# Kernel tuning notes

Measured on AMD Instinct MI355X. Metric: run time of the kernel, lower is better.

The kernel has to match this reference:

```python
import jax, jax.numpy as jnp
import numpy as np

B, N, STRIDE, NSAMPLE, RADIUS = 2, 8192, 4, 32, 0.1
CIN, COUT, LPC = 64, 128, 16
M = N // STRIDE
EPS = 1e-5


def conv1d(x, W, b=None):
    y = jnp.einsum('oc,bcn->bon', W, x)
    return y + b[None, :, None] if b is not None else y


def conv2d(x, W, b=None):
    y = jnp.einsum('oc,bcmk->bomk', W, x)
    return y + b[None, :, None, None] if b is not None else y


def bn(x, prm):
    # prm: [4, C] = (gamma, beta, running_mean, running_var); inference BN
    sh = (1, -1) + (1,) * (x.ndim - 2)
    g, be, m, v = (prm[i].reshape(sh) for i in range(4))
    return (x - m) * jax.lax.rsqrt(v + EPS) * g + be


def fps(p, m):
    # furthest point sampling, p: [B,N,3] -> idx [B,m] int32 (starts at index 0)
    b, n, _ = p.shape
    first = jnp.zeros((b,), jnp.int32)
    d0 = jnp.full((b, n), 1e10, p.dtype)

    def step(carry, _):
        dist, last = carry
        lastp = jnp.take_along_axis(p, jnp.broadcast_to(last[:, None, None], (b, 1, 3)), axis=1)
        dist = jnp.minimum(dist, jnp.sum((p - lastp) ** 2, -1))
        nxt = jnp.argmax(dist, -1).astype(jnp.int32)
        return (dist, nxt), nxt

    _, rest = jax.lax.scan(step, (d0, first), None, length=m - 1)
    return jnp.concatenate([first[:, None], rest.T], axis=1)


def ball_query(q, s, radius, ns):
    # q [B,M,3], s [B,N,3] -> neighbor indices [B,M,ns] (first ns points within radius, padded with first hit)
    n = s.shape[1]
    sqd = jnp.sum((q[:, :, None, :] - s[:, None, :, :]) ** 2, -1)  # [B,M,N]
    cand = jnp.where(sqd < radius * radius, jnp.arange(n, dtype=jnp.int32)[None, None, :], n)
    srt = jnp.sort(cand, axis=-1)[:, :, :ns]
    first = srt[:, :, :1]
    return jnp.where(srt == n, first, srt)


def group(feat, gidx):
    # feat [B,C,N], gidx [B,M,ns] -> [B,C,M,ns]
    return jax.vmap(lambda ft, gi: ft[:, gi])(feat, gidx)


def setup_inputs() -> dict:
    key = jax.random.key(0)
    ks = jax.random.split(key, 24)

    def w(k_, o, i):
        return jax.random.normal(k_, (o, i), jnp.float32) / np.sqrt(i).astype(np.float32)

    def bnp(k_, c):  # positive gamma/var, small-ish beta/mean
        return jax.random.uniform(k_, (4, c), jnp.float32) + 0.1

    return {
        'p': jax.random.uniform(ks[0], (B, N, 3), jnp.float32),
        'lp': jax.random.normal(ks[1], (B, LPC, N), jnp.float32),
        'f': jax.random.normal(ks[2], (B, CIN, N), jnp.float32),
        'W_skip': w(ks[3], COUT, CIN), 'b_skip': jax.random.normal(ks[4], (COUT,), jnp.float32) * 0.02,
        'W_post': w(ks[5], COUT, CIN), 'bn_post': bnp(ks[6], COUT),
        'W_loc1': w(ks[7], 32, LPC), 'bn_loc1': bnp(ks[8], 32),
        'W_loc2': w(ks[9], COUT, 32), 'bn_loc2': bnp(ks[10], COUT),
        'W_g': w(ks[11], 1, CIN), 'b_g': jax.random.normal(ks[12], (1,), jnp.float32) * 0.02,
        'W_v': w(ks[13], CIN, CIN), 'b_v': jax.random.normal(ks[14], (CIN,), jnp.float32) * 0.02,
        'W_w1': w(ks[15], CIN // 4, CIN), 'bn_w1': bnp(ks[16], CIN // 4),
        'W_w2': w(ks[17], CIN, CIN // 4), 'b_w2': jax.random.normal(ks[18], (CIN,), jnp.float32) * 0.02,
        'W_m': w(ks[19], COUT, CIN), 'bn_m': bnp(ks[20], COUT),
    }


def reference(p, lp, f, W_skip, b_skip, W_post, bn_post, W_loc1, bn_loc1, W_loc2, bn_loc2,
              W_g, b_g, W_v, b_v, W_w1, bn_w1, W_w2, b_w2, W_m, bn_m):
    b, n = p.shape[0], p.shape[1]
    m = n // STRIDE
    relu = jax.nn.relu

    # --- sampling + gathers ---
    idx = fps(p, m)  # [B,M]
    new_p = jnp.take_along_axis(p, jnp.broadcast_to(idx[:, :, None], (b, m, 3)), axis=1)
    fi = jnp.take_along_axis(f, jnp.broadcast_to(idx[:, None, :], (b, f.shape[1], m)), axis=2)
    lpi = jnp.take_along_axis(lp, jnp.broadcast_to(idx[:, None, :], (b, lp.shape[1], m)), axis=2)
    identity = conv1d(fi, W_skip, b_skip)  # [B,COUT,M]

    # --- global top-k relative-position attention branch ---
    att = jax.nn.sigmoid(conv1d(fi, W_g, b_g))  # [B,1,M]
    k = min(m // 4, 160)
    _, index_k = jax.lax.top_k(att[:, 0, :], k)  # [B,k]
    sparse_f = jnp.take_along_axis(fi, jnp.broadcast_to(index_k[:, None, :], (b, fi.shape[1], k)), axis=2)
    v = conv1d(sparse_f, W_v, b_v)  # [B,CIN,k]
    fi_att = fi * att
    r_qk = fi_att[:, :, :, None] - sparse_f[:, :, None, :]  # [B,CIN,M,k]
    r_qk = relu(bn(conv2d(r_qk, W_w1), bn_w1))
    r_qk = conv2d(r_qk, W_w2, b_w2)
    w_ = relu(r_qk)
    attfeat = jnp.mean(w_ * v[:, :, None, :], axis=-1)  # [B,CIN,M]
    global_f = relu(bn(conv1d(attfeat - fi, W_m), bn_m))  # [B,COUT,M]

    # --- local grouping branch ---
    fpost = relu(bn(conv1d(f, W_post), bn_post))  # [B,COUT,N]
    lpf = jnp.concatenate([lp, fpost], axis=1)  # [B,LPC+COUT,N]
    gidx = ball_query(new_p, p, RADIUS, NSAMPLE)  # [B,M,ns]
    lpfj = group(lpf, gidx)  # [B,LPC+COUT,M,ns]
    lpj, fj = lpfj[:, :LPC], lpfj[:, LPC:]
    dlpj = lpj - lpi[:, :, :, None]
    loc = relu(bn(conv2d(dlpj, W_loc1), bn_loc1))
    loc = relu(bn(conv2d(loc, W_loc2), bn_loc2))
    fout = jnp.max(fj + loc, axis=-1)  # [B,COUT,M]
    fout = fout + global_f
    fout = relu(fout + identity)
    return new_p, lpi, fout
```

## Files before the change

### kernel.cpp

```cpp
#include <hip/hip_runtime.h>
#include <stdint.h>

#define BB 2
#define NN 8192
#define MM 2048
#define CIN_ 64
#define COUT_ 128
#define LPC_ 16
#define NS_ 32
#define KSEL 160
#define EPSB 1e-5f

#define WS_IDX    0
#define WS_IDXK   4096
#define WS_LOGIT  4416
#define WS_ATT    8512
#define WS_FLAG   16380
#define WS_FIT    16384
#define WS_IDT    278528
#define WS_A1S    802816
#define WS_VT     868352
#define WS_B1S    888832
#define WS_GFT    893952
#define WS_FPOST  1418240
#define WS_GIDX   3515392

#define OUT_NEWP 0
#define OUT_LPI  12288
#define OUT_F    77824

typedef float    f16v __attribute__((ext_vector_type(16)));
typedef unsigned u16v __attribute__((ext_vector_type(16)));
typedef int      i16v __attribute__((ext_vector_type(16)));
typedef unsigned u8v  __attribute__((ext_vector_type(8)));

__device__ __forceinline__ float dist2_rn(float ax, float ay, float az,
                                          float bx, float by, float bz) {
  float dx = __fsub_rn(ax, bx);
  float dy = __fsub_rn(ay, by);
  float dz = __fsub_rn(az, bz);
  return __fadd_rn(__fadd_rn(__fmul_rn(dx, dx), __fmul_rn(dy, dy)), __fmul_rn(dz, dz));
}

template <int CTRL>
__device__ __forceinline__ unsigned long long dppmax64(unsigned long long x) {
  unsigned lo = (unsigned)x, hi = (unsigned)(x >> 32);
  unsigned plo = (unsigned)__builtin_amdgcn_update_dpp(0, (int)lo, CTRL, 0xF, 0xF, true);
  unsigned phi = (unsigned)__builtin_amdgcn_update_dpp(0, (int)hi, CTRL, 0xF, 0xF, true);
  unsigned long long o = ((unsigned long long)phi << 32) | plo;
  return o > x ? o : x;
}
#define DPP_XOR1 0xB1
#define DPP_XOR2 0x4E
#define DPP_HALFMIR 0x141
#define DPP_MIR 0x140
#define DPP_BC15 0x142
#define DPP_BC31 0x143

__device__ __forceinline__ unsigned mort4(unsigned x) {
  return (x & 1u) | ((x & 2u) << 2) | ((x & 4u) << 4) | ((x & 8u) << 6);
}

#define PPT 16
#define FPS_T 512
#define NWAVE 8
#define FPOST_BLKS ((BB * NN * 16) / FPS_T)
#define WARM_BLKS 254
#define WARM_CAP 32768
#define ANCHOR_CAP 8192

__global__ __launch_bounds__(FPS_T) void k_fps_fpost(const float* __restrict__ p,
                                                     int* __restrict__ idx_out,
                                                     const float* __restrict__ f,
                                                     const float* __restrict__ Wpost,
                                                     const float* __restrict__ bnpost,
                                                     float* __restrict__ fpostT,
                                                     int* __restrict__ flag) {
  __shared__ float2 xyl[NN];
  __shared__ union UZ {
    float zz[NN];
    struct { float zlow[NN - 4096]; unsigned short perm[NN]; } s;
  } uz;
  __shared__ union UH {
    unsigned int hist[4096];
    int idxs[MM];
  } uh;
  __shared__ unsigned long long slots[2][NWAVE];
  __shared__ unsigned int wsum[NWAVE];

  if (blockIdx.x >= 2 + FPOST_BLKS) {
    if (blockIdx.x == 2 + FPOST_BLKS) {
      float a = 1.0000001f, acc = (float)threadIdx.x;
      for (int it = 0; it < ANCHOR_CAP; ++it) {
        if (__hip_atomic_load(flag, __ATOMIC_RELAXED, __HIP_MEMORY_SCOPE_AGENT) >= 2) break;
        #pragma unroll 64
        for (int k = 0; k < 512; ++k) acc = __builtin_fmaf(acc, a, 1.0f);
      }
      asm volatile("" ::"v"(acc));
    } else {
      for (int it = 0; it < WARM_CAP; ++it) {
        if (__hip_atomic_load(flag, __ATOMIC_RELAXED, __HIP_MEMORY_SCOPE_AGENT) >= 2) break;
        __builtin_amdgcn_s_sleep(8);
      }
    }
    return;
  }

  if (blockIdx.x >= 2) {
    int gt = (blockIdx.x - 2) * FPS_T + threadIdx.x;
    int og = gt & 15, nn = gt >> 4;
    int b = nn >> 13, n = nn & 8191;
    const float* fb = f + b * CIN_ * NN + n;
    float acc[8];
    #pragma unroll
    for (int q = 0; q < 8; q++) acc[q] = 0.f;
    for (int c = 0; c < 64; c++) {
      float x = fb[c * NN];
      #pragma unroll
      for (int q = 0; q < 8; q++) acc[q] = fmaf(Wpost[(og * 8 + q) * 64 + c], x, acc[q]);
    }
    #pragma unroll
    for (int q = 0; q < 8; q++) {
      int o = og * 8 + q;
      float ga = bnpost[o], be = bnpost[COUT_ + o], mu = bnpost[2 * COUT_ + o],
            va = bnpost[3 * COUT_ + o];
      float sc = ga / sqrtf(va + EPSB);
      fpostT[(b * NN + n) * 128 + o] = fmaxf(acc[q] * sc + (be - mu * sc), 0.f);
    }
    return;
  }

  const int b = blockIdx.x;
  if (threadIdx.x == 0)
    __hip_atomic_store(flag, 0, __ATOMIC_RELAXED, __HIP_MEMORY_SCOPE_AGENT);
  const float* pb = p + b * NN * 3;
  const int tid = threadIdx.x;
  const int lane = tid & 63;
  const int wid = tid >> 6;

  for (int i = tid; i < 4096; i += FPS_T) uh.hist[i] = 0u;
  __syncthreads();

  i16v cellv;
  #pragma unroll
  for (int k = 0; k < PPT; k++) {
    int i = tid + k * FPS_T;
    float x = pb[i * 3 + 0], y = pb[i * 3 + 1], z = pb[i * 3 + 2];
    int cx = (int)(x * 16.f); cx = cx < 0 ? 0 : (cx > 15 ? 15 : cx);
    int cy = (int)(y * 16.f); cy = cy < 0 ? 0 : (cy > 15 ? 15 : cy);
    int cz = (int)(z * 16.f); cz = cz < 0 ? 0 : (cz > 15 ? 15 : cz);
    int c = (int)(mort4((unsigned)cx) | (mort4((unsigned)cy) << 1) |
                  (mort4((unsigned)cz) << 2));
    cellv[k] = c;
    atomicAdd(&uh.hist[c], 1u);
  }
  __syncthreads();

  u8v h;
  unsigned int s = 0;
  #pragma unroll
  for (int k = 0; k < 8; k++) { h[k] = uh.hist[tid * 8 + k]; s += h[k]; }
  unsigned int pre = s;
  for (int d = 1; d < 64; d <<= 1) {
    unsigned int o = (unsigned int)__shfl_up((int)pre, d);
    if (lane >= d) pre += o;
  }
  if (lane == 63) wsum[wid] = pre;
  __syncthreads();
  if (tid < NWAVE) {
    unsigned int v = wsum[tid];
    unsigned int q = v;
    for (int d = 1; d < NWAVE; d <<= 1) {
      unsigned int o = (unsigned int)__shfl_up((int)q, d);
      if (tid >= d) q += o;
    }
    wsum[tid] = q - v;
  }
  __syncthreads();
  unsigned int base = wsum[wid] + (pre - s);
  #pragma unroll
  for (int k = 0; k < 8; k++) {
    uh.hist[tid * 8 + k] = base;
    base += h[k];
  }
  __syncthreads();

  #pragma unroll
  for (int k = 0; k < PPT; k++) {
    unsigned int pos = atomicAdd(&uh.hist[cellv[k]], 1u);
    uz.s.perm[pos] = (unsigned short)(tid + k * FPS_T);
  }
  __syncthreads();

  u16v porig;
  #pragma unroll
  for (int q = 0; q < PPT; q++) porig[q] = uz.s.perm[tid * PPT + q];
  __syncthreads();

  f16v dist;
  u16v lov;
  float bxmin = 1e30f, bymin = 1e30f, bzmin = 1e30f;
  float bxmax = -1e30f, bymax = -1e30f, bzmax = -1e30f;
  #pragma unroll
  for (int q = 0; q < PPT; q++) {
    unsigned int o = porig[q];
    float x = pb[o * 3 + 0], y = pb[o * 3 + 1], z = pb[o * 3 + 2];
    xyl[q * FPS_T + tid] = make_float2(x, y);
    uz.zz[q * FPS_T + tid] = z;
    lov[q] = ((8191u - o) << 13) | ((unsigned)tid << 4) | (unsigned)q;
    dist[q] = 1e10f;
    bxmin = fminf(bxmin, x); bxmax = fmaxf(bxmax, x);
    bymin = fminf(bymin, y); bymax = fmaxf(bymax, y);
    bzmin = fminf(bzmin, z); bzmax = fmaxf(bzmax, z);
  }

  float wx = pb[0], wy = pb[1], wz = pb[2];
  unsigned long long thrPack = ((unsigned long long)__float_as_uint(1e10f) << 32);
  __syncthreads();

  if (tid == 0) uh.idxs[0] = 0;

  for (int t = 1; t < MM; t++) {
    const int buf = t & 1;
    float ex = fmaxf(fmaxf(bxmin - wx, wx - bxmax), 0.f);
    float ey = fmaxf(fmaxf(bymin - wy, wy - bymax), 0.f);
    float ez = fmaxf(fmaxf(bzmin - wz, wz - bzmax), 0.f);
    float bd = (ex * ex + ey * ey + ez * ez) * 0.999f;
    float thrMax = __uint_as_float((unsigned int)(thrPack >> 32));
    bool active = (bd < thrMax);
    if (active) {
      unsigned long long m0 = 0ull, m1 = 0ull, m2 = 0ull, m3 = 0ull;
      #pragma unroll
      for (int q = 0; q < PPT; q++) {
        float2 a = xyl[q * FPS_T + tid];
        float az = uz.zz[q * FPS_T + tid];
        float d = dist2_rn(a.x, a.y, az, wx, wy, wz);
        float nd = fminf(dist[q], d);
        dist[q] = nd;
        unsigned long long pk =
            ((unsigned long long)__float_as_uint(nd) << 32) | (unsigned long long)lov[q];
        if ((q & 3) == 0) m0 = pk > m0 ? pk : m0;
        else if ((q & 3) == 1) m1 = pk > m1 ? pk : m1;
        else if ((q & 3) == 2) m2 = pk > m2 ? pk : m2;
        else m3 = pk > m3 ? pk : m3;
      }
      unsigned long long ba = m0 > m1 ? m0 : m1;
      unsigned long long bb2 = m2 > m3 ? m2 : m3;
      thrPack = ba > bb2 ? ba : bb2;
    }
    unsigned long long wp = thrPack;
    wp = dppmax64<DPP_XOR1>(wp);
    wp = dppmax64<DPP_XOR2>(wp);
    wp = dppmax64<DPP_HALFMIR>(wp);
    wp = dppmax64<DPP_MIR>(wp);
    wp = dppmax64<DPP_BC15>(wp);
    wp = dppmax64<DPP_BC31>(wp);
    unsigned wlo = (unsigned)__builtin_amdgcn_readlane((int)(unsigned)wp, 63);
    unsigned whi = (unsigned)__builtin_amdgcn_readlane((int)(unsigned)(wp >> 32), 63);
    unsigned long long wmax = ((unsigned long long)whi << 32) | wlo;
    if (thrPack == wmax) slots[buf][wid] = wmax;
    __syncthreads();

    int sidx = lane & (NWAVE - 1);
    unsigned long long w2 = slots[buf][sidx];
    w2 = dppmax64<DPP_XOR1>(w2);
    w2 = dppmax64<DPP_XOR2>(w2);
    w2 = dppmax64<DPP_HALFMIR>(w2);
    unsigned lo32 = (unsigned)w2;
    int tidwin = (int)((lo32 >> 4) & 511u);
    int qwin = (int)(lo32 & 15u);
    float2 cw = xyl[qwin * FPS_T + tidwin];
    float zw = uz.zz[qwin * FPS_T + tidwin];
    wx = cw.x; wy = cw.y; wz = zw;
    if (tid == 0) uh.idxs[t] = 8191 - (int)((lo32 >> 13) & 0x1FFFu);
  }
  __syncthreads();

  for (int i = tid; i < MM; i += FPS_T) idx_out[b * MM + i] = uh.idxs[i];
  __syncthreads();
  if (tid == 0)
    __hip_atomic_fetch_add(flag, 1, __ATOMIC_RELEASE, __HIP_MEMORY_SCOPE_AGENT);
}

__global__ __launch_bounds__(256) void k_gather(const float* __restrict__ p,
                                                const float* __restrict__ lp,
                                                const float* __restrict__ f,
                                                const int* __restrict__ idx,
                                                const float* __restrict__ Wg,
                                                const float* __restrict__ bg,
                                                float* __restrict__ fiT,
                                                float* __restrict__ logit,
                                                float* __restrict__ att,
                                                float* __restrict__ out_lpi,
                                                float* __restrict__ out_newp) {
  int gm = blockIdx.x * 256 + threadIdx.x;
  if (gm >= BB * MM) return;
  int b = gm >> 11, m = gm & 2047;
  int j = idx[gm];
  out_newp[gm * 3 + 0] = p[(b * NN + j) * 3 + 0];
  out_newp[gm * 3 + 1] = p[(b * NN + j) * 3 + 1];
  out_newp[gm * 3 + 2] = p[(b * NN + j) * 3 + 2];
  const float* lpb = lp + b * LPC_ * NN;
  float* olpi = out_lpi + b * LPC_ * MM;
  #pragma unroll
  for (int c = 0; c < LPC_; c++) olpi[c * MM + m] = lpb[c * NN + j];
  const float* fb = f + b * CIN_ * NN;
  float lg = bg[0];
  #pragma unroll
  for (int c = 0; c < CIN_; c++) {
    float x = fb[c * NN + j];
    fiT[gm * 64 + c] = x;
    lg = __fadd_rn(lg, __fmul_rn(Wg[c], x));
  }
  logit[gm] = lg;
  att[gm] = 1.f / (1.f + expf(-lg));
}

__global__ __launch_bounds__(256) void k_ident(const float* __restrict__ fiT,
                                               const float* __restrict__ Wskip,
                                               const float* __restrict__ bskip,
                                               float* __restrict__ idT) {
  int gt = blockIdx.x * 256 + threadIdx.x;
  if (gt >= BB * MM * 16) return;
  int og = gt & 15, gm = gt >> 4;
  const float* fvp = fiT + gm * 64;
  #pragma unroll
  for (int q = 0; q < 8; q++) {
    int o = og * 8 + q;
    float a = bskip[o];
    #pragma unroll
    for (int c = 0; c < 64; c++) a = fmaf(Wskip[o * 64 + c], fvp[c], a);
    idT[gm * 128 + o] = a;
  }
}

__global__ __launch_bounds__(1024) void k_topk(const float* __restrict__ att,
                                               int* __restrict__ idxk) {
  __shared__ unsigned long long key[MM];
  int b = blockIdx.x, tid = threadIdx.x;
  for (int i = tid; i < MM; i += 1024) {
    unsigned int u = __float_as_uint(att[b * MM + i]);
    u ^= (u & 0x80000000u) ? 0xFFFFFFFFu : 0x80000000u;
    u = ~u;
    key[i] = ((unsigned long long)u << 32) | (unsigned int)i;
  }
  __syncthreads();
  for (int k = 2; k <= MM; k <<= 1) {
    for (int j = k >> 1; j > 0; j >>= 1) {
      for (int i = tid; i < MM; i += 1024) {
        int ixj = i ^ j;
        if (ixj > i) {
          bool up = (i & k) == 0;
          unsigned long long a = key[i], c = key[ixj];
          if ((a > c) == up) { key[i] = c; key[ixj] = a; }
        }
      }
      __syncthreads();
    }
  }
  if (tid < KSEL) idxk[b * KSEL + tid] = (int)(key[tid] & 0xFFFFFFFFull);
}

__global__ __launch_bounds__(256) void k_a1s(const float* __restrict__ fiT,
                                             const float* __restrict__ att,
                                             const float* __restrict__ Ww1,
                                             const float* __restrict__ bnw1,
                                             float* __restrict__ a1sT) {
  int gm = blockIdx.x * 256 + threadIdx.x;
  if (gm >= BB * MM) return;
  const float* fvp = fiT + gm * 64;
  float a = att[gm];
  #pragma unroll
  for (int c1 = 0; c1 < 16; c1++) {
    float acc = 0.f;
    #pragma unroll
    for (int c = 0; c < 64; c++) acc = fmaf(Ww1[c1 * 64 + c], fvp[c] * a, acc);
    float g = bnw1[c1], be = bnw1[16 + c1], mu = bnw1[32 + c1], va = bnw1[48 + c1];
    float sc = g / sqrtf(va + EPSB);
    a1sT[gm * 16 + c1] = acc * sc + (be - mu * sc);
  }
}

__global__ __launch_bounds__(256) void k_vb1(const float* __restrict__ fiT,
                                             const int* __restrict__ idxk,
                                             const float* __restrict__ Wv,
                                             const float* __restrict__ bv,
                                             const float* __restrict__ Ww1,
                                             const float* __restrict__ bnw1,
                                             float* __restrict__ vT,
                                             float* __restrict__ b1sT) {
  int gk = blockIdx.x * 256 + threadIdx.x;
  if (gk >= BB * KSEL) return;
  int b = gk / KSEL;
  int kk = idxk[gk];
  const float* fvp = fiT + (b * MM + kk) * 64;
  for (int o = 0; o < 64; o++) {
    float acc = bv[o];
    #pragma unroll
    for (int c = 0; c < 64; c++) acc = fmaf(Wv[o * 64 + c], fvp[c], acc);
    vT[gk * 64 + o] = acc;
  }
  #pragma unroll
  for (int c1 = 0; c1 < 16; c1++) {
    float acc = 0.f;
    #pragma unroll
    for (int c = 0; c < 64; c++) acc = fmaf(Ww1[c1 * 64 + c], fvp[c], acc);
    float g = bnw1[c1], va = bnw1[48 + c1];
    b1sT[gk * 16 + c1] = acc * (g / sqrtf(va + EPSB));
  }
}

__global__ __launch_bounds__(256) void k_att(const float* __restrict__ a1sT,
                                             const float* __restrict__ b1sT,
                                             const float* __restrict__ vT,
                                             const float* __restrict__ fiT,
                                             const float* __restrict__ Ww2,
                                             const float* __restrict__ bw2,
                                             const float* __restrict__ Wm,
                                             const float* __restrict__ bnm,
                                             float* __restrict__ gfT) {
  __shared__ float B1sh[KSEL * 16];
  __shared__ float dsh[4][64];
  int b = blockIdx.x >> 9;
  const float* bsrc = b1sT + b * KSEL * 16;
  for (int i = threadIdx.x; i < KSEL * 16; i += 256) B1sh[i] = bsrc[i];
  __syncthreads();
  int wid = threadIdx.x >> 6, lane = threadIdx.x & 63;
  int gm = blockIdx.x * 4 + wid;
  int c15 = lane & 15;
  float a1 = a1sT[gm * 16 + c15];
  f16v wrow;
  #pragma unroll
  for (int c = 0; c < 16; c++) wrow[c] = Ww2[lane * 16 + c];
  float bw = bw2[lane];
  const float* vp = vT + b * KSEL * 64 + lane;
  float acc = 0.f;
  for (int k = 0; k < KSEL; k++) {
    float t = fmaxf(a1 - B1sh[k * 16 + c15], 0.f);
    float r2 = bw;
    #pragma unroll
    for (int c = 0; c < 16; c++) {
      float tc = __int_as_float(__builtin_amdgcn_readlane(__float_as_int(t), c));
      r2 = fmaf(wrow[c], tc, r2);
    }
    acc = fmaf(fmaxf(r2, 0.f), vp[k * 64], acc);
  }
  float af = acc * (1.f / (float)KSEL);
  float d = af - fiT[gm * 64 + lane];
  dsh[wid][lane] = d;
  __syncthreads();
  #pragma unroll
  for (int t2 = 0; t2 < 2; t2++) {
    int o = lane + t2 * 64;
    float g = 0.f;
    #pragma unroll
    for (int c = 0; c < 64; c++) g = fmaf(Wm[o * 64 + c], dsh[wid][c], g);
    float ga = bnm[o], be = bnm[COUT_ + o], mu = bnm[2 * COUT_ + o], va = bnm[3 * COUT_ + o];
    float sc = ga / sqrtf(va + EPSB);
    gfT[gm * 128 + o] = fmaxf(g * sc + (be - mu * sc), 0.f);
  }
}

__global__ __launch_bounds__(256) void k_ball(const float* __restrict__ p,
                                              const float* __restrict__ newp,
                                              int* __restrict__ gidx) {
  int wid = threadIdx.x >> 6, lane = threadIdx.x & 63;
  int gm = blockIdx.x * 4 + wid;
  int b = gm >> 11;
  const float* q = newp + gm * 3;
  float qx = q[0], qy = q[1], qz = q[2];
  const float* pb = p + b * NN * 3;
  int* out = gidx + gm * NS_;
  const float RR = (float)(0.1 * 0.1);
  int cnt = 0, firstj = 0;
  bool haveFirst = false;
  for (int chunk = 0; chunk < NN / 64 && cnt < NS_; chunk++) {
    int j = chunk * 64 + lane;
    float d = dist2_rn(qx, qy, qz, pb[j * 3], pb[j * 3 + 1], pb[j * 3 + 2]);
    unsigned long long mask = __ballot(d < RR);
    while (mask && cnt < NS_) {
      int l = __ffsll(mask) - 1;
      mask &= mask - 1;
      int jj = chunk * 64 + l;
      if (!haveFirst) { firstj = jj; haveFirst = true; }
      if (lane == 0) out[cnt] = jj;
      cnt++;
    }
  }
  if (lane == 0) {
    for (int i = cnt; i < NS_; i++) out[i] = firstj;
  }
}

__global__ __launch_bounds__(128) void k_final(const float* __restrict__ lp,
                                               const float* __restrict__ lpi_out,
                                               const int* __restrict__ gidx,
                                               const float* __restrict__ Wl1,
                                               const float* __restrict__ bnl1,
                                               const float* __restrict__ Wl2,
                                               const float* __restrict__ bnl2,
                                               const float* __restrict__ fpostT,
                                               const float* __restrict__ gfT,
                                               const float* __restrict__ idT,
                                               float* __restrict__ out_f) {
  __shared__ float loc1[NS_][32];
  __shared__ float dls[NS_][16];
  int gm = blockIdx.x;
  int b = gm >> 11, m = gm & 2047;
  int tid = threadIdx.x;
  const int* gx = gidx + gm * NS_;
  for (int i = tid; i < NS_ * 16; i += 128) {
    int s = i >> 4, c = i & 15;
    int j = gx[s];
    dls[s][c] = lp[(b * LPC_ + c) * NN + j] - lpi_out[(b * LPC_ + c) * MM + m];
  }
  __syncthreads();
  for (int i = tid; i < NS_ * 32; i += 128) {
    int s = i >> 5, o = i & 31;
    float a = 0.f;
    #pragma unroll
    for (int c = 0; c < 16; c++) a = fmaf(Wl1[o * 16 + c], dls[s][c], a);
    float ga = bnl1[o], be = bnl1[32 + o], mu = bnl1[64 + o], va = bnl1[96 + o];
    float sc = ga / sqrtf(va + EPSB);
    loc1[s][o] = fmaxf(a * sc + (be - mu * sc), 0.f);
  }
  __syncthreads();
  f16v wr0, wr1;
  #pragma unroll
  for (int c = 0; c < 16; c++) { wr0[c] = Wl2[tid * 32 + c]; wr1[c] = Wl2[tid * 32 + 16 + c]; }
  float ga = bnl2[tid], be = bnl2[128 + tid], mu = bnl2[256 + tid], va = bnl2[384 + tid];
  float sc = ga / sqrtf(va + EPSB);
  float sh = be - mu * sc;
  float mx = -1e30f;
  for (int s = 0; s < NS_; s++) {
    float g = 0.f;
    #pragma unroll
    for (int c = 0; c < 16; c++) g = fmaf(wr0[c], loc1[s][c], g);
    #pragma unroll
    for (int c = 0; c < 16; c++) g = fmaf(wr1[c], loc1[s][16 + c], g);
    float l2 = fmaxf(g * sc + sh, 0.f);
    int j = gx[s];
    float fj = fpostT[(b * NN + j) * 128 + tid];
    mx = fmaxf(mx, fj + l2);
  }
  float fout = fmaxf(mx + gfT[gm * 128 + tid] + idT[gm * 128 + tid], 0.f);
  out_f[(b * COUT_ + tid) * MM + m] = fout;
}

extern "C" void kernel_launch(void* const* d_in, const int* in_sizes, int n_in,
                              void* d_out, int out_size, void* d_ws, size_t ws_size,
                              hipStream_t stream) {
  (void)in_sizes; (void)n_in; (void)out_size; (void)ws_size;
  const float* p      = (const float*)d_in[0];
  const float* lp     = (const float*)d_in[1];
  const float* f      = (const float*)d_in[2];
  const float* W_skip = (const float*)d_in[3];
  const float* b_skip = (const float*)d_in[4];
  const float* W_post = (const float*)d_in[5];
  const float* bn_post= (const float*)d_in[6];
  const float* W_loc1 = (const float*)d_in[7];
  const float* bn_loc1= (const float*)d_in[8];
  const float* W_loc2 = (const float*)d_in[9];
  const float* bn_loc2= (const float*)d_in[10];
  const float* W_g    = (const float*)d_in[11];
  const float* b_g    = (const float*)d_in[12];
  const float* W_v    = (const float*)d_in[13];
  const float* b_v    = (const float*)d_in[14];
  const float* W_w1   = (const float*)d_in[15];
  const float* bn_w1  = (const float*)d_in[16];
  const float* W_w2   = (const float*)d_in[17];
  const float* b_w2   = (const float*)d_in[18];
  const float* W_m    = (const float*)d_in[19];
  const float* bn_m   = (const float*)d_in[20];

  float* out = (float*)d_out;
  float* ws = (float*)d_ws;
  int*   idx    = (int*)(ws + WS_IDX);
  int*   idxk   = (int*)(ws + WS_IDXK);
  float* att    = ws + WS_ATT;
  int*   flag   = (int*)(ws + WS_FLAG);
  float* fiT    = ws + WS_FIT;
  float* idT    = ws + WS_IDT;
  float* a1sT   = ws + WS_A1S;
  float* vT     = ws + WS_VT;
  float* b1sT   = ws + WS_B1S;
  float* gfT    = ws + WS_GFT;
  float* fpostT = ws + WS_FPOST;
  float* logit  = ws + WS_LOGIT;
  int*   gidx   = (int*)(ws + WS_GIDX);

  k_fps_fpost<<<2 + FPOST_BLKS + WARM_BLKS, FPS_T, 0, stream>>>(p, idx, f, W_post, bn_post,
                                                                fpostT, flag);
  k_gather<<<(BB * MM + 255) / 256, 256, 0, stream>>>(p, lp, f, idx, W_g, b_g, fiT, logit, att,
                                                      out + OUT_LPI, out + OUT_NEWP);
  k_ident<<<(BB * MM * 16) / 256, 256, 0, stream>>>(fiT, W_skip, b_skip, idT);
  k_topk<<<BB, 1024, 0, stream>>>(att, idxk);
  k_a1s<<<(BB * MM + 255) / 256, 256, 0, stream>>>(fiT, att, W_w1, bn_w1, a1sT);
  k_vb1<<<(BB * KSEL + 255) / 256, 256, 0, stream>>>(fiT, idxk, W_v, b_v, W_w1, bn_w1, vT, b1sT);
  k_att<<<(BB * MM) / 4, 256, 0, stream>>>(a1sT, b1sT, vT, fiT, W_w2, b_w2, W_m, bn_m, gfT);
  k_ball<<<(BB * MM) / 4, 256, 0, stream>>>(p, out + OUT_NEWP, gidx);
  k_final<<<BB * MM, 128, 0, stream>>>(lp, out + OUT_LPI, gidx, W_loc1, bn_loc1, W_loc2, bn_loc2,
                                       fpostT, gfT, idT, out + OUT_F);
}
```

Measured before the change: 2.335 ms.

## Fuse small kernels into gather, attention and final kernels to cut launches

Folds the a1s projection into the gather kernel, the skip/identity projection into the attention kernel, and the ball query into the final kernel, so k_ident, k_a1s and k_ball disappear. It removes three launches and the round trips of idT inputs, a1s inputs and gidx through global memory. The cost is that ball query now runs inside each 128-thread final block with only one wave active during the search, and the attention kernel does more per-thread work. The a1s computation now applies att after accumulation rather than per element, which changes rounding slightly.

```diff
diff --git a/kernel.cpp b/kernel.cpp
--- a/kernel.cpp
+++ b/kernel.cpp
@@ -13,7 +13,6 @@
 
 #define WS_IDX    0
 #define WS_IDXK   4096
-#define WS_LOGIT  4416
 #define WS_ATT    8512
 #define WS_FLAG   16380
 #define WS_FIT    16384
@@ -23,7 +22,6 @@
 #define WS_B1S    888832
 #define WS_GFT    893952
 #define WS_FPOST  1418240
-#define WS_GIDX   3515392
 
 #define OUT_NEWP 0
 #define OUT_LPI  12288
@@ -288,9 +286,11 @@
                                                 const int* __restrict__ idx,
                                                 const float* __restrict__ Wg,
                                                 const float* __restrict__ bg,
+                                                const float* __restrict__ Ww1,
+                                                const float* __restrict__ bnw1,
                                                 float* __restrict__ fiT,
-                                                float* __restrict__ logit,
                                                 float* __restrict__ att,
+                                                float* __restrict__ a1sT,
                                                 float* __restrict__ out_lpi,
                                                 float* __restrict__ out_newp) {
   int gm = blockIdx.x * 256 + threadIdx.x;
@@ -306,31 +306,23 @@
   for (int c = 0; c < LPC_; c++) olpi[c * MM + m] = lpb[c * NN + j];
   const float* fb = f + b * CIN_ * NN;
   float lg = bg[0];
-  #pragma unroll
+  f16v acc;
+  #pragma unroll
+  for (int c1 = 0; c1 < 16; c1++) acc[c1] = 0.f;
   for (int c = 0; c < CIN_; c++) {
     float x = fb[c * NN + j];
     fiT[gm * 64 + c] = x;
     lg = __fadd_rn(lg, __fmul_rn(Wg[c], x));
-  }
-  logit[gm] = lg;
-  att[gm] = 1.f / (1.f + expf(-lg));
-}
-
-__global__ __launch_bounds__(256) void k_ident(const float* __restrict__ fiT,
-                                               const float* __restrict__ Wskip,
-                                               const float* __restrict__ bskip,
-                                               float* __restrict__ idT) {
-  int gt = blockIdx.x * 256 + threadIdx.x;
-  if (gt >= BB * MM * 16) return;
-  int og = gt & 15, gm = gt >> 4;
-  const float* fvp = fiT + gm * 64;
-  #pragma unroll
-  for (int q = 0; q < 8; q++) {
-    int o = og * 8 + q;
-    float a = bskip[o];
-    #pragma unroll
-    for (int c = 0; c < 64; c++) a = fmaf(Wskip[o * 64 + c], fvp[c], a);
-    idT[gm * 128 + o] = a;
+    #pragma unroll
+    for (int c1 = 0; c1 < 16; c1++) acc[c1] = fmaf(Ww1[c1 * 64 + c], x, acc[c1]);
+  }
+  float a = 1.f / (1.f + expf(-lg));
+  att[gm] = a;
+  #pragma unroll
+  for (int c1 = 0; c1 < 16; c1++) {
+    float g = bnw1[c1], be = bnw1[16 + c1], mu = bnw1[32 + c1], va = bnw1[48 + c1];
+    float sc = g / sqrtf(va + EPSB);
+    a1sT[gm * 16 + c1] = (acc[c1] * a) * sc + (be - mu * sc);
   }
 }
 
@@ -359,26 +351,6 @@
     }
   }
   if (tid < KSEL) idxk[b * KSEL + tid] = (int)(key[tid] & 0xFFFFFFFFull);
-}
-
-__global__ __launch_bounds__(256) void k_a1s(const float* __restrict__ fiT,
-                                             const float* __restrict__ att,
-                                             const float* __restrict__ Ww1,
-                                             const float* __restrict__ bnw1,
-                                             float* __restrict__ a1sT) {
-  int gm = blockIdx.x * 256 + threadIdx.x;
-  if (gm >= BB * MM) return;
-  const float* fvp = fiT + gm * 64;
-  float a = att[gm];
-  #pragma unroll
-  for (int c1 = 0; c1 < 16; c1++) {
-    float acc = 0.f;
-    #pragma unroll
-    for (int c = 0; c < 64; c++) acc = fmaf(Ww1[c1 * 64 + c], fvp[c] * a, acc);
-    float g = bnw1[c1], be = bnw1[16 + c1], mu = bnw1[32 + c1], va = bnw1[48 + c1];
-    float sc = g / sqrtf(va + EPSB);
-    a1sT[gm * 16 + c1] = acc * sc + (be - mu * sc);
-  }
 }
 
 __global__ __launch_bounds__(256) void k_vb1(const float* __restrict__ fiT,
@@ -418,9 +390,13 @@
                                              const float* __restrict__ bw2,
                                              const float* __restrict__ Wm,
                                              const float* __restrict__ bnm,
-                                             float* __restrict__ gfT) {
+                                             const float* __restrict__ Wskip,
+                                             const float* __restrict__ bskip,
+                                             float* __restrict__ gfT,
+                                             float* __restrict__ idT) {
   __shared__ float B1sh[KSEL * 16];
   __shared__ float dsh[4][64];
+  __shared__ float fish[4][64];
   int b = blockIdx.x >> 9;
   const float* bsrc = b1sT + b * KSEL * 16;
   for (int i = threadIdx.x; i < KSEL * 16; i += 256) B1sh[i] = bsrc[i];
@@ -429,6 +405,8 @@
   int gm = blockIdx.x * 4 + wid;
   int c15 = lane & 15;
   float a1 = a1sT[gm * 16 + c15];
+  float fval = fiT[gm * 64 + lane];
+  fish[wid][lane] = fval;
   f16v wrow;
   #pragma unroll
   for (int c = 0; c < 16; c++) wrow[c] = Ww2[lane * 16 + c];
@@ -446,55 +424,29 @@
     acc = fmaf(fmaxf(r2, 0.f), vp[k * 64], acc);
   }
   float af = acc * (1.f / (float)KSEL);
-  float d = af - fiT[gm * 64 + lane];
+  float d = af - fval;
   dsh[wid][lane] = d;
   __syncthreads();
   #pragma unroll
   for (int t2 = 0; t2 < 2; t2++) {
     int o = lane + t2 * 64;
     float g = 0.f;
+    float ida = bskip[o];
     #pragma unroll
     for (int c = 0; c < 64; c++) g = fmaf(Wm[o * 64 + c], dsh[wid][c], g);
+    #pragma unroll
+    for (int c = 0; c < 64; c++) ida = fmaf(Wskip[o * 64 + c], fish[wid][c], ida);
     float ga = bnm[o], be = bnm[COUT_ + o], mu = bnm[2 * COUT_ + o], va = bnm[3 * COUT_ + o];
     float sc = ga / sqrtf(va + EPSB);
     gfT[gm * 128 + o] = fmaxf(g * sc + (be - mu * sc), 0.f);
-  }
-}
-
-__global__ __launch_bounds__(256) void k_ball(const float* __restrict__ p,
-                                              const float* __restrict__ newp,
-                                              int* __restrict__ gidx) {
-  int wid = threadIdx.x >> 6, lane = threadIdx.x & 63;
-  int gm = blockIdx.x * 4 + wid;
-  int b = gm >> 11;
-  const float* q = newp + gm * 3;
-  float qx = q[0], qy = q[1], qz = q[2];
-  const float* pb = p + b * NN * 3;
-  int* out = gidx + gm * NS_;
-  const float RR = (float)(0.1 * 0.1);
-  int cnt = 0, firstj = 0;
-  bool haveFirst = false;
-  for (int chunk = 0; chunk < NN / 64 && cnt < NS_; chunk++) {
-    int j = chunk * 64 + lane;
-    float d = dist2_rn(qx, qy, qz, pb[j * 3], pb[j * 3 + 1], pb[j * 3 + 2]);
-    unsigned long long mask = __ballot(d < RR);
-    while (mask && cnt < NS_) {
-      int l = __ffsll(mask) - 1;
-      mask &= mask - 1;
-      int jj = chunk * 64 + l;
-      if (!haveFirst) { firstj = jj; haveFirst = true; }
-      if (lane == 0) out[cnt] = jj;
-      cnt++;
-    }
-  }
-  if (lane == 0) {
-    for (int i = cnt; i < NS_; i++) out[i] = firstj;
-  }
-}
-
-__global__ __launch_bounds__(128) void k_final(const float* __restrict__ lp,
+    idT[gm * 128 + o] = ida;
+  }
+}
+
+__global__ __launch_bounds__(128) void k_final(const float* __restrict__ p,
+                                               const float* __restrict__ newp,
+                                               const float* __restrict__ lp,
                                                const float* __restrict__ lpi_out,
-                                               const int* __restrict__ gidx,
                                                const float* __restrict__ Wl1,
                                                const float* __restrict__ bnl1,
                                                const float* __restrict__ Wl2,
@@ -505,13 +457,40 @@
                                                float* __restrict__ out_f) {
   __shared__ float loc1[NS_][32];
   __shared__ float dls[NS_][16];
+  __shared__ int gxs[NS_];
   int gm = blockIdx.x;
   int b = gm >> 11, m = gm & 2047;
   int tid = threadIdx.x;
-  const int* gx = gidx + gm * NS_;
+
+  if (tid < 64) {
+    int lane = tid;
+    float qx = newp[gm * 3 + 0], qy = newp[gm * 3 + 1], qz = newp[gm * 3 + 2];
+    const float* pb = p + b * NN * 3;
+    const float RR = (float)(0.1 * 0.1);
+    int cnt = 0, firstj = 0;
+    bool haveFirst = false;
+    for (int chunk = 0; chunk < NN / 64 && cnt < NS_; chunk++) {
+      int j = chunk * 64 + lane;
+      float d = dist2_rn(qx, qy, qz, pb[j * 3], pb[j * 3 + 1], pb[j * 3 + 2]);
+      unsigned long long mask = __ballot(d < RR);
+      while (mask && cnt < NS_) {
+        int l = __ffsll(mask) - 1;
+        mask &= mask - 1;
+        int jj = chunk * 64 + l;
+        if (!haveFirst) { firstj = jj; haveFirst = true; }
+        if (lane == 0) gxs[cnt] = jj;
+        cnt++;
+      }
+    }
+    if (lane == 0) {
+      for (int i = cnt; i < NS_; i++) gxs[i] = firstj;
+    }
+  }
+  __syncthreads();
+
   for (int i = tid; i < NS_ * 16; i += 128) {
     int s = i >> 4, c = i & 15;
-    int j = gx[s];
+    int j = gxs[s];
     dls[s][c] = lp[(b * LPC_ + c) * NN + j] - lpi_out[(b * LPC_ + c) * MM + m];
   }
   __syncthreads();
@@ -539,7 +518,7 @@
     #pragma unroll
     for (int c = 0; c < 16; c++) g = fmaf(wr1[c], loc1[s][16 + c], g);
     float l2 = fmaxf(g * sc + sh, 0.f);
-    int j = gx[s];
+    int j = gxs[s];
     float fj = fpostT[(b * NN + j) * 128 + tid];
     mx = fmaxf(mx, fj + l2);
   }
@@ -586,19 +565,16 @@
   float* b1sT   = ws + WS_B1S;
   float* gfT    = ws + WS_GFT;
   float* fpostT = ws + WS_FPOST;
-  float* logit  = ws + WS_LOGIT;
-  int*   gidx   = (int*)(ws + WS_GIDX);
 
   k_fps_fpost<<<2 + FPOST_BLKS + WARM_BLKS, FPS_T, 0, stream>>>(p, idx, f, W_post, bn_post,
                                                                 fpostT, flag);
-  k_gather<<<(BB * MM + 255) / 256, 256, 0, stream>>>(p, lp, f, idx, W_g, b_g, fiT, logit, att,
-                                                      out + OUT_LPI, out + OUT_NEWP);
-  k_ident<<<(BB * MM * 16) / 256, 256, 0, stream>>>(fiT, W_skip, b_skip, idT);
+  k_gather<<<(BB * MM + 255) / 256, 256, 0, stream>>>(p, lp, f, idx, W_g, b_g, W_w1, bn_w1,
+                                                      fiT, att, a1sT, out + OUT_LPI,
+                                                      out + OUT_NEWP);
   k_topk<<<BB, 1024, 0, stream>>>(att, idxk);
-  k_a1s<<<(BB * MM + 255) / 256, 256, 0, stream>>>(fiT, att, W_w1, bn_w1, a1sT);
   k_vb1<<<(BB * KSEL + 255) / 256, 256, 0, stream>>>(fiT, idxk, W_v, b_v, W_w1, bn_w1, vT, b1sT);
-  k_att<<<(BB * MM) / 4, 256, 0, stream>>>(a1sT, b1sT, vT, fiT, W_w2, b_w2, W_m, bn_m, gfT);
-  k_ball<<<(BB * MM) / 4, 256, 0, stream>>>(p, out + OUT_NEWP, gidx);
-  k_final<<<BB * MM, 128, 0, stream>>>(lp, out + OUT_LPI, gidx, W_loc1, bn_loc1, W_loc2, bn_loc2,
-                                       fpostT, gfT, idT, out + OUT_F);
-}
+  k_att<<<(BB * MM) / 4, 256, 0, stream>>>(a1sT, b1sT, vT, fiT, W_w2, b_w2, W_m, bn_m,
+                                           W_skip, b_skip, gfT, idT);
+  k_final<<<BB * MM, 128, 0, stream>>>(p, out + OUT_NEWP, lp, out + OUT_LPI, W_loc1, bn_loc1,
+                                       W_loc2, bn_loc2, fpostT, gfT, idT, out + OUT_F);
+}
```

Result: no change. 2.332 ms (-0.1%).
